# Kernel tuning notes

Hardware: AMD Instinct MI355X
Metric: run time of the kernel (lower is better)

## Reference

```python
import jax, jax.numpy as jnp
import numpy as np

N, M, K, CIN, COUT = 65536, 16385, 16, 256, 512
RATIO = 0.25
LN_EPS = 1e-5


def setup_inputs() -> dict:
    key = jax.random.key(0)
    k0, k1, k2, k3, k4 = jax.random.split(key, 5)
    xyz = jax.random.normal(k0, (N, 3), dtype=jnp.float32)
    feats = jax.random.normal(k1, (N, CIN), dtype=jnp.float32)
    samp_idx = jax.random.randint(k2, (M,), 0, N, dtype=jnp.int32)
    knn_idx = jax.random.randint(k3, (M, K), 0, N, dtype=jnp.int32)
    norm_w = jnp.ones((CIN,), dtype=jnp.float32)
    norm_b = jnp.zeros((CIN,), dtype=jnp.float32)
    lin_w = jax.random.normal(k4, (COUT, CIN), dtype=jnp.float32) * (1.0 / np.sqrt(CIN))
    return {"xyz": xyz, "feats": feats, "norm_w": norm_w, "norm_b": norm_b,
            "lin_w": lin_w, "samp_idx": samp_idx, "knn_idx": knn_idx, "offset": N}


def reference(xyz, feats, norm_w, norm_b, lin_w, samp_idx, knn_idx, offset):
    # n_offset = int(offset * ratio) + 1 (single point cloud)
    m = int(offset * RATIO) + 1
    n_offset = jnp.array([m], dtype=jnp.int32)
    # FPS output -> sampled coordinates
    n_xyz = xyz[samp_idx]                                  # [m, 3]
    # queryandgroup(use_xyz=False): gather k-NN neighbor features
    g = feats[knn_idx]                                     # [m, k, cin]
    # LayerNorm over channel dim
    mu = jnp.mean(g, axis=-1, keepdims=True)
    var = jnp.mean(jnp.square(g - mu), axis=-1, keepdims=True)
    normed = (g - mu) * jax.lax.rsqrt(var + LN_EPS) * norm_w + norm_b
    # bias-free Linear cin -> cout
    proj = jnp.einsum('mkc,oc->mko', normed, lin_w)        # [m, k, cout]
    # MaxPool1d over the k neighbors
    out = jnp.max(proj, axis=1)                            # [m, cout]
    return n_xyz, out, n_offset
```

## Files before the change

kernel.cpp:

```cpp
#include <hip/hip_runtime.h>

#define M_PTS   16385
#define K_NB    16
#define CIN_C   256
#define COUT_C  512
#define LN_EPS  1e-5f

#define OUT_XYZ_ELEMS (M_PTS * 3)
#define OUT_FEAT_OFF  OUT_XYZ_ELEMS
#define OUT_NOFF_IDX  (OUT_XYZ_ELEMS + M_PTS * COUT_C)

#define NBLK 256
#define PPB  65

#define B_SCALE 16.0f
#define B_INV   0.0625f

#define AROW_B 272

typedef __attribute__((ext_vector_type(4))) float f32x4;

__device__ __forceinline__ void block_sync_lds() {
  asm volatile("s_waitcnt lgkmcnt(0)" ::: "memory");
  __builtin_amdgcn_s_barrier();
}

__device__ __forceinline__ float wave_sum64(float v) {
  v += __int_as_float(__builtin_amdgcn_update_dpp(0, __float_as_int(v), 0xB1, 0xF, 0xF, false));
  v += __int_as_float(__builtin_amdgcn_update_dpp(0, __float_as_int(v), 0x4E, 0xF, 0xF, false));
  v += __int_as_float(__builtin_amdgcn_update_dpp(0, __float_as_int(v), 0x141, 0xF, 0xF, false));
  v += __int_as_float(__builtin_amdgcn_update_dpp(0, __float_as_int(v), 0x140, 0xF, 0xF, false));
  v += __int_as_float(__builtin_amdgcn_update_dpp(0, __float_as_int(v), 0x142, 0xA, 0xF, false));
  v += __int_as_float(__builtin_amdgcn_update_dpp(0, __float_as_int(v), 0x143, 0xC, 0xF, false));
  return __int_as_float(__builtin_amdgcn_readlane(__float_as_int(v), 63));
}

__device__ __forceinline__ int ln_pack(float4 g, float4 nw, float4 nb) {
  float s1 = (g.x + g.y) + (g.z + g.w);
  float s2 = g.x * g.x + g.y * g.y + g.z * g.z + g.w * g.w;
  float S1 = wave_sum64(s1);
  float S2 = wave_sum64(s2);
  float mu  = S1 * (1.0f / 256.0f);
  float var = fmaf(-mu, mu, S2 * (1.0f / 256.0f));
  float rs  = rsqrtf(var + LN_EPS);
  float a = fmaf((g.x - mu) * rs, nw.x, nb.x);
  float b = fmaf((g.y - mu) * rs, nw.y, nb.y);
  float c = fmaf((g.z - mu) * rs, nw.z, nb.z);
  float d = fmaf((g.w - mu) * rs, nw.w, nb.w);
  int v = __builtin_amdgcn_cvt_pk_fp8_f32(a, b, 0, false);
  v = __builtin_amdgcn_cvt_pk_fp8_f32(c, d, v, true);
  return v;
}

__global__ void prep_kernel(const float* __restrict__ lin_w,
                            const float* __restrict__ xyz,
                            const int*   __restrict__ samp_idx,
                            const int*   __restrict__ offset,
                            unsigned char* __restrict__ lw8,
                            float*  __restrict__ out) {
  int tid = blockIdx.x * 256 + threadIdx.x;
  if (tid < COUT_C * CIN_C) {
    int o = tid >> 8;
    int c = tid & 255;
    int pos = ((o >> 5) << 13) | (((o >> 4) & 1) << 12) | ((c >> 5) << 9)
            | ((((c >> 3) & 3) * 16 + (o & 15)) << 3) | (c & 7);
    int pk = __builtin_amdgcn_cvt_pk_fp8_f32(lin_w[tid] * B_SCALE, 0.0f, 0, false);
    lw8[pos] = (unsigned char)(pk & 0xFF);
  }
  if (tid < OUT_XYZ_ELEMS) {
    int p = tid / 3;
    int c = tid - p * 3;
    out[tid] = xyz[(size_t)samp_idx[p] * 3 + c];
  }
  if (tid == 0) out[OUT_NOFF_IDX] = (float)(offset[0] / 4 + 1);
}

__device__ __forceinline__ void gemm_pool(const unsigned char* rowbase,
                                          const long Breg[8][2], int quad,
                                          float& v0, float& v1) {
  ulonglong2 q0 = *(const ulonglong2*)(rowbase + 0   + quad * 16);
  ulonglong2 q1 = *(const ulonglong2*)(rowbase + 64  + quad * 16);
  ulonglong2 q2 = *(const ulonglong2*)(rowbase + 128 + quad * 16);
  ulonglong2 q3 = *(const ulonglong2*)(rowbase + 192 + quad * 16);
  f32x4 a0 = {0.f, 0.f, 0.f, 0.f}, a1 = {0.f, 0.f, 0.f, 0.f};
  a0 = __builtin_amdgcn_mfma_f32_16x16x32_fp8_fp8((long)q0.x, Breg[0][0], a0, 0, 0, 0);
  a1 = __builtin_amdgcn_mfma_f32_16x16x32_fp8_fp8((long)q0.x, Breg[0][1], a1, 0, 0, 0);
  a0 = __builtin_amdgcn_mfma_f32_16x16x32_fp8_fp8((long)q0.y, Breg[1][0], a0, 0, 0, 0);
  a1 = __builtin_amdgcn_mfma_f32_16x16x32_fp8_fp8((long)q0.y, Breg[1][1], a1, 0, 0, 0);
  a0 = __builtin_amdgcn_mfma_f32_16x16x32_fp8_fp8((long)q1.x, Breg[2][0], a0, 0, 0, 0);
  a1 = __builtin_amdgcn_mfma_f32_16x16x32_fp8_fp8((long)q1.x, Breg[2][1], a1, 0, 0, 0);
  a0 = __builtin_amdgcn_mfma_f32_16x16x32_fp8_fp8((long)q1.y, Breg[3][0], a0, 0, 0, 0);
  a1 = __builtin_amdgcn_mfma_f32_16x16x32_fp8_fp8((long)q1.y, Breg[3][1], a1, 0, 0, 0);
  a0 = __builtin_amdgcn_mfma_f32_16x16x32_fp8_fp8((long)q2.x, Breg[4][0], a0, 0, 0, 0);
  a1 = __builtin_amdgcn_mfma_f32_16x16x32_fp8_fp8((long)q2.x, Breg[4][1], a1, 0, 0, 0);
  a0 = __builtin_amdgcn_mfma_f32_16x16x32_fp8_fp8((long)q2.y, Breg[5][0], a0, 0, 0, 0);
  a1 = __builtin_amdgcn_mfma_f32_16x16x32_fp8_fp8((long)q2.y, Breg[5][1], a1, 0, 0, 0);
  a0 = __builtin_amdgcn_mfma_f32_16x16x32_fp8_fp8((long)q3.x, Breg[6][0], a0, 0, 0, 0);
  a1 = __builtin_amdgcn_mfma_f32_16x16x32_fp8_fp8((long)q3.x, Breg[6][1], a1, 0, 0, 0);
  a0 = __builtin_amdgcn_mfma_f32_16x16x32_fp8_fp8((long)q3.y, Breg[7][0], a0, 0, 0, 0);
  a1 = __builtin_amdgcn_mfma_f32_16x16x32_fp8_fp8((long)q3.y, Breg[7][1], a1, 0, 0, 0);
  v0 = fmaxf(fmaxf(a0[0], a0[1]), fmaxf(a0[2], a0[3]));
  v0 = fmaxf(v0, __shfl_xor(v0, 16, 64));
  v0 = fmaxf(v0, __shfl_xor(v0, 32, 64));
  v1 = fmaxf(fmaxf(a1[0], a1[1]), fmaxf(a1[2], a1[3]));
  v1 = fmaxf(v1, __shfl_xor(v1, 16, 64));
  v1 = fmaxf(v1, __shfl_xor(v1, 32, 64));
}

__global__ __launch_bounds__(1024, 4)
void td_main(const float*  __restrict__ feats,
             const float*  __restrict__ norm_w,
             const float*  __restrict__ norm_b,
             const unsigned char* __restrict__ lw8,
             const int*    __restrict__ knn,
             float* __restrict__ out) {
  __shared__ unsigned char A8[2][32 * AROW_B];
  __shared__ int Kidx[PPB * K_NB];

  const int tid  = threadIdx.x;
  const int lane = tid & 63;
  const int w    = tid >> 6;
  const int quad = lane >> 4;
  const int lcol = lane & 15;

  const int pstart = blockIdx.x * PPB;
  const int npts   = min(pstart + PPB, M_PTS) - pstart;
  if (npts <= 0) return;

  for (int i = tid; i < npts * K_NB; i += 1024)
    Kidx[i] = knn[pstart * K_NB + i];

  long Breg[8][2];
  {
    const unsigned char* base = lw8 + (w << 13) + lane * 8;
#pragma unroll
    for (int g = 0; g < 2; ++g)
#pragma unroll
      for (int kk = 0; kk < 8; ++kk) {
        Breg[kk][g] = *(const long*)(base + (g << 12) + (kk << 9));
        asm volatile("" : "+v"(Breg[kk][g]));
      }
  }

  const float4 nw = ((const float4*)norm_w)[lane];
  const float4 nb = ((const float4*)norm_b)[lane];

  const int wdw = ((lane >> 4) << 6) + (((lane >> 1) & 3) << 4)
                + (lane & 8) + ((lane & 1) << 2);

  __syncthreads();

  float4 fa = ((const float4*)(feats + (size_t)Kidx[w] * CIN_C))[lane];
  float4 fb = ((const float4*)(feats +
               (size_t)Kidx[min(1, npts - 1) * K_NB + w] * CIN_C))[lane];

  const int nit = (npts + 1) >> 1;
  for (int it = 0; it < nit; ++it) {
    const int pa = 2 * it, pb = 2 * it + 1;

    float4 na = fa, nb2 = fb;
    if (it + 1 < nit) {
      int qa = min(pa + 2, npts - 1), qb = min(pa + 3, npts - 1);
      na  = ((const float4*)(feats + (size_t)Kidx[qa * K_NB + w] * CIN_C))[lane];
      nb2 = ((const float4*)(feats + (size_t)Kidx[qb * K_NB + w] * CIN_C))[lane];
    }

    unsigned char* Ab = A8[it & 1];
    *(int*)(Ab + w * AROW_B + wdw)        = ln_pack(fa, nw, nb);
    *(int*)(Ab + (16 + w) * AROW_B + wdw) = ln_pack(fb, nw, nb);

    block_sync_lds();

    float v0, v1;
    gemm_pool(Ab + lcol * AROW_B, Breg, quad, v0, v1);
    float* outa = out + OUT_FEAT_OFF + (size_t)(pstart + pa) * COUT_C + w * 32;
    if (quad < 2) outa[quad * 16 + lcol] = (quad ? v1 : v0) * B_INV;

    gemm_pool(Ab + (16 + lcol) * AROW_B, Breg, quad, v0, v1);
    if (pb < npts) {
      float* outb = out + OUT_FEAT_OFF + (size_t)(pstart + pb) * COUT_C + w * 32;
      if (quad < 2) outb[quad * 16 + lcol] = (quad ? v1 : v0) * B_INV;
    }
    fa = na; fb = nb2;
  }
}

extern "C" void kernel_launch(void* const* d_in, const int* in_sizes, int n_in,
                              void* d_out, int out_size, void* d_ws, size_t ws_size,
                              hipStream_t stream) {
  const float* xyz      = (const float*)d_in[0];
  const float* feats    = (const float*)d_in[1];
  const float* norm_w   = (const float*)d_in[2];
  const float* norm_b   = (const float*)d_in[3];
  const float* lin_w    = (const float*)d_in[4];
  const int*   samp_idx = (const int*)d_in[5];
  const int*   knn      = (const int*)d_in[6];
  const int*   offset   = (const int*)d_in[7];
  float* out = (float*)d_out;
  unsigned char* lw8 = (unsigned char*)d_ws;

  prep_kernel<<<512, 256, 0, stream>>>(lin_w, xyz, samp_idx, offset, lw8, out);

  td_main<<<NBLK, 1024, 0, stream>>>(feats, norm_w, norm_b, lw8, knn, out);
}
```

Measured before the change: 178.6 us.

## Precompute LayerNorm+fp8 table per input row, stream rows into LDS asynchronously

Instead of normalizing each gathered neighbor row (256 floats, 16x redundantly across M*K gathers), a prep pass now normalizes all N input rows once and stores them as fp8 in a pre-swizzled 256-byte table. The main kernel gathers those compact rows straight into LDS with global_load_lds and a 4-deep buffer ring managed by explicit vmcnt waits. Points per block drop to 32 and the grid grows to 513 blocks. This cuts gather bandwidth and the per-gather reduction work, at the cost of an extra full pass over feats plus a table write, and it relies on the hand-counted vmcnt bookkeeping being right.

```diff
diff --git a/kernel.cpp b/kernel.cpp
--- a/kernel.cpp
+++ b/kernel.cpp
@@ -4,14 +4,18 @@
 #define K_NB    16
 #define CIN_C   256
 #define COUT_C  512
+#define N_ROWS  65536
 #define LN_EPS  1e-5f
 
 #define OUT_XYZ_ELEMS (M_PTS * 3)
 #define OUT_FEAT_OFF  OUT_XYZ_ELEMS
 #define OUT_NOFF_IDX  (OUT_XYZ_ELEMS + M_PTS * COUT_C)
 
-#define NBLK 256
-#define PPB  65
+#define LN_BLOCKS   (N_ROWS / 4)
+#define PREP_BLOCKS 512
+
+#define NBLK 513
+#define PPB  32
 
 #define B_SCALE 16.0f
 #define B_INV   0.0625f
@@ -19,11 +23,6 @@
 #define AROW_B 272
 
 typedef __attribute__((ext_vector_type(4))) float f32x4;
-
-__device__ __forceinline__ void block_sync_lds() {
-  asm volatile("s_waitcnt lgkmcnt(0)" ::: "memory");
-  __builtin_amdgcn_s_barrier();
-}
 
 __device__ __forceinline__ float wave_sum64(float v) {
   v += __int_as_float(__builtin_amdgcn_update_dpp(0, __float_as_int(v), 0xB1, 0xF, 0xF, false));
@@ -52,13 +51,33 @@
   return v;
 }
 
+__device__ __forceinline__ int wdw_of(int lane) {
+  return ((lane >> 4) << 6) + (((lane >> 1) & 3) << 4)
+       + (lane & 8) + ((lane & 1) << 2);
+}
+
 __global__ void prep_kernel(const float* __restrict__ lin_w,
                             const float* __restrict__ xyz,
+                            const float* __restrict__ feats,
+                            const float* __restrict__ norm_w,
+                            const float* __restrict__ norm_b,
                             const int*   __restrict__ samp_idx,
                             const int*   __restrict__ offset,
                             unsigned char* __restrict__ lw8,
+                            unsigned char* __restrict__ tab,
                             float*  __restrict__ out) {
-  int tid = blockIdx.x * 256 + threadIdx.x;
+  int bx = blockIdx.x;
+  if (bx < LN_BLOCKS) {
+    int lane = threadIdx.x & 63;
+    int row  = (bx << 2) + (threadIdx.x >> 6);
+    float4 g  = ((const float4*)(feats + (size_t)row * CIN_C))[lane];
+    float4 nw = ((const float4*)norm_w)[lane];
+    float4 nb = ((const float4*)norm_b)[lane];
+    int pk = ln_pack(g, nw, nb);
+    *(int*)(tab + ((size_t)row << 8) + wdw_of(lane)) = pk;
+    return;
+  }
+  int tid = (bx - LN_BLOCKS) * 256 + threadIdx.x;
   if (tid < COUT_C * CIN_C) {
     int o = tid >> 8;
     int c = tid & 255;
@@ -73,6 +92,15 @@
     out[tid] = xyz[(size_t)samp_idx[p] * 3 + c];
   }
   if (tid == 0) out[OUT_NOFF_IDX] = (float)(offset[0] / 4 + 1);
+}
+
+__device__ __forceinline__ void load_row(const unsigned char* __restrict__ tab,
+                                         int idx, unsigned char* ldsrow, int lane) {
+  const unsigned char* src = tab + ((size_t)(unsigned)idx << 8) + (lane << 2);
+  __builtin_amdgcn_global_load_lds(
+      (const __attribute__((address_space(1))) unsigned int*)src,
+      (__attribute__((address_space(3))) unsigned int*)ldsrow,
+      4, 0, 0);
 }
 
 __device__ __forceinline__ void gemm_pool(const unsigned char* rowbase,
@@ -107,14 +135,12 @@
   v1 = fmaxf(v1, __shfl_xor(v1, 32, 64));
 }
 
-__global__ __launch_bounds__(1024, 4)
-void td_main(const float*  __restrict__ feats,
-             const float*  __restrict__ norm_w,
-             const float*  __restrict__ norm_b,
+__global__ __launch_bounds__(1024, 8)
+void td_main(const unsigned char* __restrict__ tab,
              const unsigned char* __restrict__ lw8,
              const int*    __restrict__ knn,
              float* __restrict__ out) {
-  __shared__ unsigned char A8[2][32 * AROW_B];
+  __shared__ __align__(16) unsigned char A8[4][2][16][AROW_B];
   __shared__ int Kidx[PPB * K_NB];
 
   const int tid  = threadIdx.x;
@@ -142,34 +168,33 @@
       }
   }
 
-  const float4 nw = ((const float4*)norm_w)[lane];
-  const float4 nb = ((const float4*)norm_b)[lane];
-
-  const int wdw = ((lane >> 4) << 6) + (((lane >> 1) & 3) << 4)
-                + (lane & 8) + ((lane & 1) << 2);
-
   __syncthreads();
 
-  float4 fa = ((const float4*)(feats + (size_t)Kidx[w] * CIN_C))[lane];
-  float4 fb = ((const float4*)(feats +
-               (size_t)Kidx[min(1, npts - 1) * K_NB + w] * CIN_C))[lane];
+  load_row(tab, Kidx[w],                                &A8[0][0][w][0], lane);
+  load_row(tab, Kidx[min(1, npts - 1) * K_NB + w],      &A8[0][1][w][0], lane);
 
   const int nit = (npts + 1) >> 1;
   for (int it = 0; it < nit; ++it) {
     const int pa = 2 * it, pb = 2 * it + 1;
 
-    float4 na = fa, nb2 = fb;
     if (it + 1 < nit) {
       int qa = min(pa + 2, npts - 1), qb = min(pa + 3, npts - 1);
-      na  = ((const float4*)(feats + (size_t)Kidx[qa * K_NB + w] * CIN_C))[lane];
-      nb2 = ((const float4*)(feats + (size_t)Kidx[qb * K_NB + w] * CIN_C))[lane];
+      int b = (it + 1) & 3;
+      load_row(tab, Kidx[qa * K_NB + w], &A8[b][0][w][0], lane);
+      load_row(tab, Kidx[qb * K_NB + w], &A8[b][1][w][0], lane);
     }
 
-    unsigned char* Ab = A8[it & 1];
-    *(int*)(Ab + w * AROW_B + wdw)        = ln_pack(fa, nw, nb);
-    *(int*)(Ab + (16 + w) * AROW_B + wdw) = ln_pack(fb, nw, nb);
-
-    block_sync_lds();
+    if (it == 0) {
+      if (nit > 1) asm volatile("s_waitcnt vmcnt(2)" ::: "memory");
+      else         asm volatile("s_waitcnt vmcnt(0)" ::: "memory");
+    } else if (it + 1 < nit) {
+      asm volatile("s_waitcnt vmcnt(4)" ::: "memory");
+    } else {
+      asm volatile("s_waitcnt vmcnt(2)" ::: "memory");
+    }
+    __builtin_amdgcn_s_barrier();
+
+    const unsigned char* Ab = &A8[it & 3][0][0][0];
 
     float v0, v1;
     gemm_pool(Ab + lcol * AROW_B, Breg, quad, v0, v1);
@@ -181,7 +206,6 @@
       float* outb = out + OUT_FEAT_OFF + (size_t)(pstart + pb) * COUT_C + w * 32;
       if (quad < 2) outb[quad * 16 + lcol] = (quad ? v1 : v0) * B_INV;
     }
-    fa = na; fb = nb2;
   }
 }
 
@@ -198,8 +222,10 @@
   const int*   offset   = (const int*)d_in[7];
   float* out = (float*)d_out;
   unsigned char* lw8 = (unsigned char*)d_ws;
-
-  prep_kernel<<<512, 256, 0, stream>>>(lin_w, xyz, samp_idx, offset, lw8, out);
-
-  td_main<<<NBLK, 1024, 0, stream>>>(feats, norm_w, norm_b, lw8, knn, out);
-}
+  unsigned char* tab = (unsigned char*)d_ws + (1 << 17);
+
+  prep_kernel<<<LN_BLOCKS + PREP_BLOCKS, 256, 0, stream>>>(
+      lin_w, xyz, feats, norm_w, norm_b, samp_idx, offset, lw8, tab, out);
+
+  td_main<<<NBLK, 1024, 0, stream>>>(tab, lw8, knn, out);
+}
```

New measurement: 161.5 us. 9.5% less time.
